# Kernel optimization log

Hardware: AMD Instinct MI355X
Metric: run time of the kernel (lower is better)

The kernel has to match this reference:

```python
import jax, jax.numpy as jnp
import numpy as np
import math

QUERY_LEN = 64
VALUES_LEN = 64
NUM_HEADS = 16


def setup_inputs() -> dict:
    key = jax.random.key(0)
    k1, k2, k3, k4 = jax.random.split(key, 4)
    B, G, N = 2, 4, 1024
    D = QUERY_LEN * NUM_HEADS  # 1024
    queries = jax.random.normal(k1, (B, G, N, D), dtype=jnp.float32)
    keys = jax.random.normal(k2, (B, G, N, D), dtype=jnp.float32)
    values = jax.random.normal(k3, (B, G, N, VALUES_LEN * NUM_HEADS), dtype=jnp.float32)
    neuron_bank_connectivity_sub = jax.random.uniform(k4, (1, G, 1, N, N), dtype=jnp.float32)
    return {
        "queries": queries,
        "keys": keys,
        "values": values,
        "neuron_bank_connectivity_sub": neuron_bank_connectivity_sub,
    }


def reference(queries, keys, values, neuron_bank_connectivity_sub):
    B, G, N, _ = queries.shape
    H, dq, dv = NUM_HEADS, QUERY_LEN, VALUES_LEN
    # view last dim as (vec_len, num_heads), move heads forward: [B,G,H,N,d]
    q = queries.reshape(B, G, N, dq, H).transpose(0, 1, 4, 2, 3)
    k = keys.reshape(B, G, N, dq, H).transpose(0, 1, 4, 2, 3)
    v = values.reshape(B, G, N, dv, H).transpose(0, 1, 4, 2, 3)
    scores = jnp.einsum('bghnd,bghmd->bghnm', q, k) / math.sqrt(dq)
    probs = jax.nn.softmax(scores - neuron_bank_connectivity_sub, axis=-1)
    out = jnp.einsum('bghnm,bghmd->bghnd', probs, v)  # [B,G,H,N,dv]
    # Faithful to original: view() applied to the contiguous [B,G,H,N,dv] buffer
    return out.reshape(B, G, N, H * dv)
```

## Files before the change

### kernel.cpp

```cpp
#include <hip/hip_runtime.h>
#include <hip/hip_bf16.h>
#include <math.h>

#define B_ 2
#define G_ 4
#define N_ 1024
#define H_ 16
#define D_ 64
#define BG_ (B_*G_)
#define BGH_ (B_*G_*H_)
#define MK 64
#define LOG2E 1.44269504f
#define QSCALE (0.125f * LOG2E)

typedef __bf16 bf16;
typedef bf16 bf16x8 __attribute__((ext_vector_type(8)));
typedef bf16 bf16x2 __attribute__((ext_vector_type(2)));
typedef float f32x4 __attribute__((ext_vector_type(4)));
typedef float f32x16 __attribute__((ext_vector_type(16)));
typedef int i32x4 __attribute__((ext_vector_type(4)));
typedef unsigned u32x2 __attribute__((ext_vector_type(2)));

static __device__ __forceinline__ f32x16 mfma32(bf16x8 a, bf16x8 b, f32x16 c) {
    return __builtin_amdgcn_mfma_f32_32x32x16_bf16(a, b, c, 0, 0, 0);
}

static __device__ __forceinline__ unsigned pk2(float a, float b) {
    bf16x2 t; t[0] = (bf16)a; t[1] = (bf16)b;
    return __builtin_bit_cast(unsigned, t);
}

static __device__ __forceinline__ void pl32swap(unsigned& a, unsigned& b, int hi) {
#if __has_builtin(__builtin_amdgcn_permlane32_swap)
    u32x2 r = __builtin_amdgcn_permlane32_swap(a, b, false, false);
    a = r[0]; b = r[1];
    (void)hi;
#else
    unsigned ax = (unsigned)__shfl_xor((int)a, 32, 64);
    unsigned bx = (unsigned)__shfl_xor((int)b, 32, 64);
    unsigned na = hi ? bx : a;
    unsigned nb = hi ? b : ax;
    a = na; b = nb;
#endif
}

static __device__ __forceinline__ void gll16(const void* gsrc, void* ldst, int lane) {
#if __has_builtin(__builtin_amdgcn_global_load_lds)
    (void)lane;
    __builtin_amdgcn_global_load_lds((const __attribute__((address_space(1))) void*)gsrc,
                                     (__attribute__((address_space(3))) void*)ldst, 16, 0, 0);
#else
    *(bf16x8*)((bf16*)ldst + lane * 8) = *(const bf16x8*)((const bf16*)gsrc);
#endif
}

#define HS 1160
#define NS 72

__global__ __launch_bounds__(256) void transpose_fused(
    const float* __restrict__ q, const float* __restrict__ k, const float* __restrict__ v,
    const float* __restrict__ bias,
    bf16* __restrict__ qt, bf16* __restrict__ ktb, bf16* __restrict__ vtT16,
    float* __restrict__ biasX)
{
    __shared__ __attribute__((aligned(16))) bf16 lds[16 * HS];
    int bx = blockIdx.x;
    int t = threadIdx.x;

    if (bx >= 3 * 512) {
        int idx = bx - 3 * 512;
        int gg  = idx >> 8;
        int tl  = idx & 255;
        int q0  = (tl >> 4) * 64;
        int m0  = (tl & 15) * 64;
        float* ldsF = (float*)lds;

        int mi = t & 15, qr = t >> 4;
#pragma unroll
        for (int rr = 0; rr < 4; ++rr) {
            int row = qr + rr * 16;
            f32x4 val = *(const f32x4*)(bias + ((size_t)(gg * N_ + q0 + row) * N_ + m0 + 4 * mi));
            *(f32x4*)(&ldsF[row * 68 + 4 * mi]) = val;
        }
        __syncthreads();
        int qr2 = t & 63, mb0 = t >> 6;
#pragma unroll
        for (int kk = 0; kk < 4; ++kk) {
            int mbi = mb0 + kk * 4;
            f32x4 vv = *(const f32x4*)(&ldsF[qr2 * 68 + 4 * mbi]);
            *(f32x4*)(biasX + (((size_t)gg * 256 + m0 / 4 + mbi) * N_ + q0 + qr2) * 4) = vv;
        }
        return;
    }

    int tensor = bx >> 9;
    int rr = bx & 511;
    int bg = rr >> 6;
    int tile = rr & 63;
    int n0 = tile * 16;

    const float* src = (tensor == 0) ? q : (tensor == 1) ? k : v;
    float scale = (tensor == 0) ? QSCALE : 1.0f;
    const float* sb = src + (size_t)bg * N_ * 1024 + (size_t)n0 * 1024;

    int h0 = 4 * (t & 3);
    int d  = t >> 2;
    int wbase = h0 * HS + d;
#pragma unroll 4
    for (int i = 0; i < 16; ++i) {
        float4 val = ((const float4*)(sb + (size_t)i * 1024))[t];
        bf16* p = &lds[wbase + i * NS];
        p[0]        = (bf16)(val.x * scale);
        p[HS]       = (bf16)(val.y * scale);
        p[2 * HS]   = (bf16)(val.z * scale);
        p[3 * HS]   = (bf16)(val.w * scale);
    }
    __syncthreads();

    if (tensor < 2) {
        bf16* dst = (tensor == 0) ? qt : ktb;
        int n  = (t >> 3) & 15;
        int db = t & 7;
        int hb = t >> 7;
#pragma unroll
        for (int i = 0; i < 8; ++i) {
            int h = 2 * i + hb;
            bf16x8 vv = *(const bf16x8*)(&lds[h * HS + n * NS + db * 8]);
            *(bf16x8*)(dst + (((size_t)(bg * H_ + h)) * N_ + n0 + n) * D_ + db * 8) = vv;
        }
    } else {
        int dd = t & 63;
        int hb = t >> 6;
#pragma unroll
        for (int i = 0; i < 4; ++i) {
            int h = hb * 4 + i;
            bf16x8 v0, v1;
#pragma unroll
            for (int jj = 0; jj < 8; ++jj) v0[jj] = lds[h * HS + jj * NS + dd];
#pragma unroll
            for (int jj = 0; jj < 8; ++jj) v1[jj] = lds[h * HS + (8 + jj) * NS + dd];
            bf16* dst = vtT16 + (((size_t)(bg * H_ + h) * 64 + tile) * D_ + dd) * 16;
            *(bf16x8*)dst       = v0;
            *(bf16x8*)(dst + 8) = v1;
        }
    }
}

__global__ __launch_bounds__(256, 2) void flash_kernel(
    const bf16* __restrict__ qt, const bf16* __restrict__ kt, const bf16* __restrict__ vtT16,
    const float* __restrict__ biasX, float* __restrict__ out)
{
    __shared__ __attribute__((aligned(16))) bf16 k_lds[2][MK][D_];
    __shared__ __attribute__((aligned(16))) bf16 v_lds[2][D_][MK];

    int tid  = threadIdx.x;
    int w    = tid >> 6;
    int lane = tid & 63;
    int hi   = lane >> 5;
    int q31  = lane & 31;
    int key8 = (q31 & 7) << 3;
    int hi8  = hi << 3;

    int wg   = blockIdx.x;
    int xcd  = wg & 7;
    int slot = wg >> 3;
    int bgh  = xcd * 16 + (slot >> 2);
    int n0   = (slot & 3) * 256;
    int g    = (bgh >> 4) & (G_ - 1);

    int qbase = n0 + w * 64;

    const bf16* qb_base = qt + ((size_t)bgh * N_ + qbase + q31) * D_ + hi * 8;
    bf16x8 qA[4], qB[4];
#pragma unroll
    for (int c = 0; c < 4; ++c) {
        qA[c] = *(const bf16x8*)(qb_base + c * 16);
        qB[c] = *(const bf16x8*)(qb_base + 32 * D_ + c * 16);
    }

    f32x16 acc00 = {0,0,0,0,0,0,0,0,0,0,0,0,0,0,0,0};
    f32x16 acc01 = {0,0,0,0,0,0,0,0,0,0,0,0,0,0,0,0};
    f32x16 acc10 = {0,0,0,0,0,0,0,0,0,0,0,0,0,0,0,0};
    f32x16 acc11 = {0,0,0,0,0,0,0,0,0,0,0,0,0,0,0,0};
    float l0 = 0.f, l1 = 0.f;

    int rloc = lane >> 3;
    int c16  = lane & 7;
    int csw  = c16 ^ rloc;
    bool isK = (w < 2);
    int wrow = (w & 1) * 32;
    const bf16* ksrc = kt + (size_t)bgh * N_ * D_ + (size_t)(wrow + rloc) * D_ + csw * 8;
    const bf16* vsrc = vtT16 + (((size_t)bgh * 64 + (csw >> 1)) * D_ + (wrow + rloc)) * 16 + (csw & 1) * 8;

    const float* bb = biasX + (size_t)g * (256u * 4096) + (size_t)(qbase + q31) * 4;

    if (isK) {
#pragma unroll
        for (int i = 0; i < 4; ++i) gll16(ksrc + (size_t)i * 8 * D_, &k_lds[0][wrow + i * 8][0], lane);
    } else {
#pragma unroll
        for (int i = 0; i < 4; ++i) gll16(vsrc + (size_t)i * 128, &v_lds[0][wrow + i * 8][0], lane);
    }
    f32x4 bv[2][4];
#pragma unroll
    for (int g01 = 0; g01 < 2; ++g01)
#pragma unroll
        for (int u = 0; u < 4; ++u)
            bv[g01][u] = *(const f32x4*)(bb + g01 * 128 + (size_t)(2 * u + hi) * 4096);

    for (int it = 0; it < N_ / MK; ++it) {
        int  cur  = it & 1;
        bool more = (it + 1 < N_ / MK);
        __syncthreads();

        if (more) {
            int nxt = cur ^ 1;
            if (isK) {
                const bf16* ks = ksrc + (size_t)(it + 1) * MK * D_;
#pragma unroll
                for (int i = 0; i < 4; ++i) gll16(ks + (size_t)i * 8 * D_, &k_lds[nxt][wrow + i * 8][0], lane);
            } else {
                const bf16* vs = vsrc + (size_t)(it + 1) * 4096;
#pragma unroll
                for (int i = 0; i < 4; ++i) gll16(vs + (size_t)i * 128, &v_lds[nxt][wrow + i * 8][0], lane);
            }
        }

        {
            f32x16 s0 = {0,0,0,0,0,0,0,0,0,0,0,0,0,0,0,0};
            f32x16 s1 = {0,0,0,0,0,0,0,0,0,0,0,0,0,0,0,0};
            __builtin_amdgcn_s_setprio(1);
#pragma unroll
            for (int c = 0; c < 4; ++c) {
                int off = ((c << 4) | hi8) ^ key8;
                bf16x8 kb = *(const bf16x8*)(&k_lds[cur][q31][off]);
                s0 = mfma32(kb, qA[c], s0);
                s1 = mfma32(kb, qB[c], s1);
            }
            __builtin_amdgcn_s_setprio(0);

            unsigned wa[2][4], wb[2][4];
#pragma unroll
            for (int g01 = 0; g01 < 2; ++g01) {
#pragma unroll
                for (int u = 0; u < 4; ++u) {
                    const f32x16& s = g01 ? s1 : s0;
                    f32x4 bvv = bv[g01][u];
                    float p0 = __builtin_amdgcn_exp2f(__builtin_fmaf(-LOG2E, bvv[0], s[4*u+0]));
                    float p1 = __builtin_amdgcn_exp2f(__builtin_fmaf(-LOG2E, bvv[1], s[4*u+1]));
                    float p2 = __builtin_amdgcn_exp2f(__builtin_fmaf(-LOG2E, bvv[2], s[4*u+2]));
                    float p3 = __builtin_amdgcn_exp2f(__builtin_fmaf(-LOG2E, bvv[3], s[4*u+3]));
                    if (g01) l1 += (p0 + p1) + (p2 + p3); else l0 += (p0 + p1) + (p2 + p3);
                    wa[g01][u] = pk2(p0, p1);
                    wb[g01][u] = pk2(p2, p3);
                }
            }

#pragma unroll
            for (int g01 = 0; g01 < 2; ++g01)
#pragma unroll
                for (int u = 0; u < 4; ++u)
                    bv[g01][u] = *(const f32x4*)(bb + g01 * 128 + (size_t)(it * 16 + 8 + 2 * u + hi) * 4096);

#pragma unroll
            for (int g01 = 0; g01 < 2; ++g01) {
                pl32swap(wa[g01][0], wa[g01][1], hi);
                pl32swap(wb[g01][0], wb[g01][1], hi);
                pl32swap(wa[g01][2], wa[g01][3], hi);
                pl32swap(wb[g01][2], wb[g01][3], hi);
            }

            __builtin_amdgcn_s_setprio(1);
#pragma unroll
            for (int c01 = 0; c01 < 2; ++c01) {
                int off = ((c01 << 4) | hi8) ^ key8;
                bf16x8 va0 = *(const bf16x8*)(&v_lds[cur][q31][off]);
                bf16x8 va1 = *(const bf16x8*)(&v_lds[cur][32 + q31][off]);
                i32x4 b0 = { (int)wa[0][2*c01], (int)wb[0][2*c01], (int)wa[0][2*c01+1], (int)wb[0][2*c01+1] };
                i32x4 b1 = { (int)wa[1][2*c01], (int)wb[1][2*c01], (int)wa[1][2*c01+1], (int)wb[1][2*c01+1] };
                bf16x8 pb0 = __builtin_bit_cast(bf16x8, b0);
                bf16x8 pb1 = __builtin_bit_cast(bf16x8, b1);
                acc00 = mfma32(va0, pb0, acc00);
                acc01 = mfma32(va1, pb0, acc01);
                acc10 = mfma32(va0, pb1, acc10);
                acc11 = mfma32(va1, pb1, acc11);
            }
            __builtin_amdgcn_s_setprio(0);
        }

        {
            f32x16 s0 = {0,0,0,0,0,0,0,0,0,0,0,0,0,0,0,0};
            f32x16 s1 = {0,0,0,0,0,0,0,0,0,0,0,0,0,0,0,0};
            __builtin_amdgcn_s_setprio(1);
#pragma unroll
            for (int c = 0; c < 4; ++c) {
                int off = ((c << 4) | hi8) ^ key8;
                bf16x8 kb = *(const bf16x8*)(&k_lds[cur][32 + q31][off]);
                s0 = mfma32(kb, qA[c], s0);
                s1 = mfma32(kb, qB[c], s1);
            }
            __builtin_amdgcn_s_setprio(0);

            unsigned wa[2][4], wb[2][4];
#pragma unroll
            for (int g01 = 0; g01 < 2; ++g01) {
#pragma unroll
                for (int u = 0; u < 4; ++u) {
                    const f32x16& s = g01 ? s1 : s0;
                    f32x4 bvv = bv[g01][u];
                    float p0 = __builtin_amdgcn_exp2f(__builtin_fmaf(-LOG2E, bvv[0], s[4*u+0]));
                    float p1 = __builtin_amdgcn_exp2f(__builtin_fmaf(-LOG2E, bvv[1], s[4*u+1]));
                    float p2 = __builtin_amdgcn_exp2f(__builtin_fmaf(-LOG2E, bvv[2], s[4*u+2]));
                    float p3 = __builtin_amdgcn_exp2f(__builtin_fmaf(-LOG2E, bvv[3], s[4*u+3]));
                    if (g01) l1 += (p0 + p1) + (p2 + p3); else l0 += (p0 + p1) + (p2 + p3);
                    wa[g01][u] = pk2(p0, p1);
                    wb[g01][u] = pk2(p2, p3);
                }
            }

            if (more) {
#pragma unroll
                for (int g01 = 0; g01 < 2; ++g01)
#pragma unroll
                    for (int u = 0; u < 4; ++u)
                        bv[g01][u] = *(const f32x4*)(bb + g01 * 128 + (size_t)((it + 1) * 16 + 2 * u + hi) * 4096);
            }

#pragma unroll
            for (int g01 = 0; g01 < 2; ++g01) {
                pl32swap(wa[g01][0], wa[g01][1], hi);
                pl32swap(wb[g01][0], wb[g01][1], hi);
                pl32swap(wa[g01][2], wa[g01][3], hi);
                pl32swap(wb[g01][2], wb[g01][3], hi);
            }

            __builtin_amdgcn_s_setprio(1);
#pragma unroll
            for (int c01 = 0; c01 < 2; ++c01) {
                int off = (((2 + c01) << 4) | hi8) ^ key8;
                bf16x8 va0 = *(const bf16x8*)(&v_lds[cur][q31][off]);
                bf16x8 va1 = *(const bf16x8*)(&v_lds[cur][32 + q31][off]);
                i32x4 b0 = { (int)wa[0][2*c01], (int)wb[0][2*c01], (int)wa[0][2*c01+1], (int)wb[0][2*c01+1] };
                i32x4 b1 = { (int)wa[1][2*c01], (int)wb[1][2*c01], (int)wa[1][2*c01+1], (int)wb[1][2*c01+1] };
                bf16x8 pb0 = __builtin_bit_cast(bf16x8, b0);
                bf16x8 pb1 = __builtin_bit_cast(bf16x8, b1);
                acc00 = mfma32(va0, pb0, acc00);
                acc01 = mfma32(va1, pb0, acc01);
                acc10 = mfma32(va0, pb1, acc10);
                acc11 = mfma32(va1, pb1, acc11);
            }
            __builtin_amdgcn_s_setprio(0);
        }
    }

    l0 += __shfl_xor(l0, 32, 64);
    l1 += __shfl_xor(l1, 32, 64);
    float inv0 = 1.0f / l0, inv1 = 1.0f / l1;

#pragma unroll
    for (int g01 = 0; g01 < 2; ++g01) {
        float inv = g01 ? inv1 : inv0;
        float* ob = out + ((size_t)bgh * N_ + qbase + g01 * 32 + q31) * D_ + hi * 4;
#pragma unroll
        for (int td = 0; td < 2; ++td) {
            const f32x16& a = g01 ? (td ? acc11 : acc10) : (td ? acc01 : acc00);
#pragma unroll
            for (int u = 0; u < 4; ++u) {
                f32x4 o = { a[4*u+0] * inv, a[4*u+1] * inv, a[4*u+2] * inv, a[4*u+3] * inv };
                *(f32x4*)(ob + td * 32 + u * 8) = o;
            }
        }
    }
}

__global__ __launch_bounds__(256) void naive_kernel(
    const float* __restrict__ q, const float* __restrict__ k,
    const float* __restrict__ v, const float* __restrict__ bias,
    float* __restrict__ out)
{
    __shared__ float sc[N_];
    __shared__ float red[256];
    __shared__ float qrow[64];
    int n = blockIdx.x;
    int bgh = blockIdx.y;
    int bg = bgh >> 4, h = bgh & 15;
    int g = bg & (G_ - 1);
    int tid = threadIdx.x;
    const float* qr = q + ((size_t)(bg * N_ + n)) * 1024;
    if (tid < 64) qrow[tid] = qr[tid * 16 + h];
    __syncthreads();
    const float* bb = bias + (size_t)g * N_ * N_ + (size_t)n * N_;
    for (int m = tid; m < N_; m += 256) {
        const float* kr = k + ((size_t)(bg * N_ + m)) * 1024 + h;
        float dot = 0.f;
        for (int d = 0; d < 64; ++d) dot += qrow[d] * kr[d * 16];
        sc[m] = dot * 0.125f - bb[m];
    }
    __syncthreads();
    float mx = -INFINITY;
    for (int m = tid; m < N_; m += 256) mx = fmaxf(mx, sc[m]);
    red[tid] = mx; __syncthreads();
    for (int s = 128; s > 0; s >>= 1) {
        if (tid < s) red[tid] = fmaxf(red[tid], red[tid + s]);
        __syncthreads();
    }
    float M = red[0]; __syncthreads();
    float sum = 0.f;
    for (int m = tid; m < N_; m += 256) { float e = __expf(sc[m] - M); sc[m] = e; sum += e; }
    red[tid] = sum; __syncthreads();
    for (int s = 128; s > 0; s >>= 1) {
        if (tid < s) red[tid] += red[tid + s];
        __syncthreads();
    }
    float L = red[0]; __syncthreads();
    int d = tid & 63, quarter = tid >> 6;
    float acc = 0.f;
    const float* vb = v + (size_t)bg * N_ * 1024 + d * 16 + h;
    for (int m = quarter * 256; m < quarter * 256 + 256; ++m) acc += sc[m] * vb[(size_t)m * 1024];
    red[tid] = acc; __syncthreads();
    if (tid < 64) {
        float o = (red[tid] + red[tid + 64] + red[tid + 128] + red[tid + 192]) / L;
        out[((size_t)bgh * N_ + n) * 64 + d] = o;
    }
}

extern "C" void kernel_launch(void* const* d_in, const int* in_sizes, int n_in,
                              void* d_out, int out_size, void* d_ws, size_t ws_size,
                              hipStream_t stream) {
    const float* q    = (const float*)d_in[0];
    const float* k    = (const float*)d_in[1];
    const float* v    = (const float*)d_in[2];
    const float* bias = (const float*)d_in[3];
    float* out = (float*)d_out;

    const size_t elems = (size_t)BGH_ * N_ * D_;
    const size_t needA = 3 * elems * sizeof(bf16);
    const size_t need  = needA + (size_t)G_ * N_ * N_ * 4;

    if (ws_size >= need) {
        bf16* qt    = (bf16*)d_ws;
        bf16* ktb   = qt + elems;
        bf16* vtT16 = ktb + elems;
        float* biasX = (float*)((char*)d_ws + needA);
        transpose_fused<<<3 * 512 + 1024, 256, 0, stream>>>(q, k, v, bias, qt, ktb, vtT16, biasX);
        flash_kernel<<<dim3(512), 256, 0, stream>>>(qt, ktb, vtT16, biasX, out);
    } else {
        dim3 grid(N_, BGH_);
        naive_kernel<<<grid, 256, 0, stream>>>(q, k, v, bias, out);
    }
}
```

Before: 207.6 us.

## Stagger per-wave half-tile order, relax barrier waitcnt, remap workgroup indices

Waves 2-3 now process the two 32-key halves of each K/V tile in the opposite order to waves 0-1, and the bias prefetch indices are adjusted to match. The aim is to spread LDS bank and exp pressure across waves so they do not all contend on the same rows at once. The full __syncthreads is replaced by an inline s_waitcnt vmcnt(8) plus s_barrier, so outstanding bias loads no longer have to drain at each iteration. The block-to-(bgh, n0) mapping is also changed to interleave heads within each XCD slot, which alters L2 reuse of K/V. The partial vmcnt relies on exact load counts for correctness of the LDS double buffer.

```diff
diff --git a/kernel.cpp b/kernel.cpp
--- a/kernel.cpp
+++ b/kernel.cpp
@@ -160,12 +160,13 @@
     int q31  = lane & 31;
     int key8 = (q31 & 7) << 3;
     int hi8  = hi << 3;
+    int flip = (w >> 1) & 1;
 
     int wg   = blockIdx.x;
     int xcd  = wg & 7;
     int slot = wg >> 3;
-    int bgh  = xcd * 16 + (slot >> 2);
-    int n0   = (slot & 3) * 256;
+    int bgh  = xcd * 16 + (slot & 15);
+    int n0   = (slot >> 4) * 256;
     int g    = (bgh >> 4) & (G_ - 1);
 
     int qbase = n0 + w * 64;
@@ -206,12 +207,13 @@
     for (int g01 = 0; g01 < 2; ++g01)
 #pragma unroll
         for (int u = 0; u < 4; ++u)
-            bv[g01][u] = *(const f32x4*)(bb + g01 * 128 + (size_t)(2 * u + hi) * 4096);
+            bv[g01][u] = *(const f32x4*)(bb + g01 * 128 + (size_t)(flip * 8 + 2 * u + hi) * 4096);
 
     for (int it = 0; it < N_ / MK; ++it) {
         int  cur  = it & 1;
         bool more = (it + 1 < N_ / MK);
-        __syncthreads();
+        asm volatile("s_waitcnt vmcnt(8)\n\ts_barrier" ::: "memory");
+        __builtin_amdgcn_sched_barrier(0);
 
         if (more) {
             int nxt = cur ^ 1;
@@ -226,14 +228,18 @@
             }
         }
 
-        {
+#pragma unroll
+        for (int ph = 0; ph < 2; ++ph) {
+            int h    = ph ^ flip;
+            int rowb = h << 5;
+
             f32x16 s0 = {0,0,0,0,0,0,0,0,0,0,0,0,0,0,0,0};
             f32x16 s1 = {0,0,0,0,0,0,0,0,0,0,0,0,0,0,0,0};
             __builtin_amdgcn_s_setprio(1);
 #pragma unroll
             for (int c = 0; c < 4; ++c) {
                 int off = ((c << 4) | hi8) ^ key8;
-                bf16x8 kb = *(const bf16x8*)(&k_lds[cur][q31][off]);
+                bf16x8 kb = *(const bf16x8*)(&k_lds[cur][rowb + q31][off]);
                 s0 = mfma32(kb, qA[c], s0);
                 s1 = mfma32(kb, qB[c], s1);
             }
@@ -256,11 +262,21 @@
                 }
             }
 
-#pragma unroll
-            for (int g01 = 0; g01 < 2; ++g01)
-#pragma unroll
-                for (int u = 0; u < 4; ++u)
-                    bv[g01][u] = *(const f32x4*)(bb + g01 * 128 + (size_t)(it * 16 + 8 + 2 * u + hi) * 4096);
+            if (ph == 0) {
+                int mbase = it * 16 + (1 ^ flip) * 8;
+#pragma unroll
+                for (int g01 = 0; g01 < 2; ++g01)
+#pragma unroll
+                    for (int u = 0; u < 4; ++u)
+                        bv[g01][u] = *(const f32x4*)(bb + g01 * 128 + (size_t)(mbase + 2 * u + hi) * 4096);
+            } else if (more) {
+                int mbase = (it + 1) * 16 + flip * 8;
+#pragma unroll
+                for (int g01 = 0; g01 < 2; ++g01)
+#pragma unroll
+                    for (int u = 0; u < 4; ++u)
+                        bv[g01][u] = *(const f32x4*)(bb + g01 * 128 + (size_t)(mbase + 2 * u + hi) * 4096);
+            }
 
 #pragma unroll
             for (int g01 = 0; g01 < 2; ++g01) {
@@ -273,71 +289,7 @@
             __builtin_amdgcn_s_setprio(1);
 #pragma unroll
             for (int c01 = 0; c01 < 2; ++c01) {
-                int off = ((c01 << 4) | hi8) ^ key8;
-                bf16x8 va0 = *(const bf16x8*)(&v_lds[cur][q31][off]);
-                bf16x8 va1 = *(const bf16x8*)(&v_lds[cur][32 + q31][off]);
-                i32x4 b0 = { (int)wa[0][2*c01], (int)wb[0][2*c01], (int)wa[0][2*c01+1], (int)wb[0][2*c01+1] };
-                i32x4 b1 = { (int)wa[1][2*c01], (int)wb[1][2*c01], (int)wa[1][2*c01+1], (int)wb[1][2*c01+1] };
-                bf16x8 pb0 = __builtin_bit_cast(bf16x8, b0);
-                bf16x8 pb1 = __builtin_bit_cast(bf16x8, b1);
-                acc00 = mfma32(va0, pb0, acc00);
-                acc01 = mfma32(va1, pb0, acc01);
-                acc10 = mfma32(va0, pb1, acc10);
-                acc11 = mfma32(va1, pb1, acc11);
-            }
-            __builtin_amdgcn_s_setprio(0);
-        }
-
-        {
-            f32x16 s0 = {0,0,0,0,0,0,0,0,0,0,0,0,0,0,0,0};
-            f32x16 s1 = {0,0,0,0,0,0,0,0,0,0,0,0,0,0,0,0};
-            __builtin_amdgcn_s_setprio(1);
-#pragma unroll
-            for (int c = 0; c < 4; ++c) {
-                int off = ((c << 4) | hi8) ^ key8;
-                bf16x8 kb = *(const bf16x8*)(&k_lds[cur][32 + q31][off]);
-                s0 = mfma32(kb, qA[c], s0);
-                s1 = mfma32(kb, qB[c], s1);
-            }
-            __builtin_amdgcn_s_setprio(0);
-
-            unsigned wa[2][4], wb[2][4];
-#pragma unroll
-            for (int g01 = 0; g01 < 2; ++g01) {
-#pragma unroll
-                for (int u = 0; u < 4; ++u) {
-                    const f32x16& s = g01 ? s1 : s0;
-                    f32x4 bvv = bv[g01][u];
-                    float p0 = __builtin_amdgcn_exp2f(__builtin_fmaf(-LOG2E, bvv[0], s[4*u+0]));
-                    float p1 = __builtin_amdgcn_exp2f(__builtin_fmaf(-LOG2E, bvv[1], s[4*u+1]));
-                    float p2 = __builtin_amdgcn_exp2f(__builtin_fmaf(-LOG2E, bvv[2], s[4*u+2]));
-                    float p3 = __builtin_amdgcn_exp2f(__builtin_fmaf(-LOG2E, bvv[3], s[4*u+3]));
-                    if (g01) l1 += (p0 + p1) + (p2 + p3); else l0 += (p0 + p1) + (p2 + p3);
-                    wa[g01][u] = pk2(p0, p1);
-                    wb[g01][u] = pk2(p2, p3);
-                }
-            }
-
-            if (more) {
-#pragma unroll
-                for (int g01 = 0; g01 < 2; ++g01)
-#pragma unroll
-                    for (int u = 0; u < 4; ++u)
-                        bv[g01][u] = *(const f32x4*)(bb + g01 * 128 + (size_t)((it + 1) * 16 + 2 * u + hi) * 4096);
-            }
-
-#pragma unroll
-            for (int g01 = 0; g01 < 2; ++g01) {
-                pl32swap(wa[g01][0], wa[g01][1], hi);
-                pl32swap(wb[g01][0], wb[g01][1], hi);
-                pl32swap(wa[g01][2], wa[g01][3], hi);
-                pl32swap(wb[g01][2], wb[g01][3], hi);
-            }
-
-            __builtin_amdgcn_s_setprio(1);
-#pragma unroll
-            for (int c01 = 0; c01 < 2; ++c01) {
-                int off = (((2 + c01) << 4) | hi8) ^ key8;
+                int off = (((2 * h + c01) << 4) | hi8) ^ key8;
                 bf16x8 va0 = *(const bf16x8*)(&v_lds[cur][q31][off]);
                 bf16x8 va1 = *(const bf16x8*)(&v_lds[cur][32 + q31][off]);
                 i32x4 b0 = { (int)wa[0][2*c01], (int)wb[0][2*c01], (int)wa[0][2*c01+1], (int)wb[0][2*c01+1] };
```

New measurement: 219.3 us. 5.6% more time.
